# Kernel tuning notes

Hardware: AMD Instinct MI355X
Metric: run time of the kernel (lower is better)

## Reference

```python
import jax, jax.numpy as jnp
import numpy as np

B, S, D_IN, D_OUT, H = 4, 2048, 1024, 1024, 16
HD = D_OUT // H


def setup_inputs() -> dict:
    key = jax.random.key(0)
    ks = jax.random.split(key, 6)
    s_in = 1.0 / np.sqrt(D_IN)
    s_out = 1.0 / np.sqrt(D_OUT)
    return {
        "x": jax.random.normal(ks[0], (B, S, D_IN), dtype=jnp.float32),
        "W_q": jax.random.uniform(ks[1], (D_OUT, D_IN), jnp.float32, -s_in, s_in),
        "W_k": jax.random.uniform(ks[2], (D_OUT, D_IN), jnp.float32, -s_in, s_in),
        "W_v": jax.random.uniform(ks[3], (D_OUT, D_IN), jnp.float32, -s_in, s_in),
        "W_o": jax.random.uniform(ks[4], (D_OUT, D_OUT), jnp.float32, -s_out, s_out),
        "b_o": jax.random.uniform(ks[5], (D_OUT,), jnp.float32, -s_out, s_out),
    }


def reference(x, W_q, W_k, W_v, W_o, b_o):
    b, s, _ = x.shape
    # torch Linear: y = x @ W.T  (no qkv bias)
    q = (x @ W_q.T).reshape(b, s, H, HD).transpose(0, 2, 1, 3)  # [b,h,s,hd]
    k = (x @ W_k.T).reshape(b, s, H, HD).transpose(0, 2, 1, 3)
    v = (x @ W_v.T).reshape(b, s, H, HD).transpose(0, 2, 1, 3)
    scores = jnp.einsum("bhqd,bhkd->bhqk", q, k)  # [b,h,s,s]
    causal = jnp.triu(jnp.ones((s, s), dtype=bool), k=1)
    scores = jnp.where(causal, -jnp.inf, scores)
    attn = jax.nn.softmax(scores / np.sqrt(HD), axis=-1)
    # dropout p=0.0 -> identity
    ctx = jnp.einsum("bhqk,bhkd->bhqd", attn, v)  # [b,h,s,hd]
    ctx = ctx.transpose(0, 2, 1, 3).reshape(b, s, D_OUT)
    return ctx @ W_o.T + b_o
```

## Files before the change

### kernel.cpp

```cpp
#include <hip/hip_runtime.h>
#include <cstdint>
#include <cstddef>

#define S_LEN  2048
#define NHEAD  16
#define HDIM   64
#define KD     1024
#define BSROWS 8192

typedef __attribute__((ext_vector_type(4))) float          floatx4;
typedef __attribute__((ext_vector_type(8))) __bf16         bf16x8;
typedef __attribute__((ext_vector_type(8))) unsigned short ushort8v;
typedef __attribute__((ext_vector_type(4))) unsigned short ushort4v;
typedef __attribute__((ext_vector_type(4))) float          float4v;

__device__ __forceinline__ unsigned short f2bf(float f) {
  unsigned int u = __float_as_uint(f);
  u += 0x7fffu + ((u >> 16) & 1u);
  return (unsigned short)(u >> 16);
}

#if __has_builtin(__builtin_amdgcn_exp2f)
#define EXP2F(x) __builtin_amdgcn_exp2f(x)
#else
#define EXP2F(x) exp2f(x)
#endif

__device__ __forceinline__ unsigned int pack2bf(float a, float b) {
#if __has_builtin(__builtin_amdgcn_perm)
  return __builtin_amdgcn_perm(__float_as_uint(b), __float_as_uint(a), 0x07060302);
#else
  return (__float_as_uint(a) >> 16) | (__float_as_uint(b) & 0xffff0000u);
#endif
}

__device__ __forceinline__ void async_cp16(const void* gsrc, void* ldst) {
  __builtin_amdgcn_global_load_lds(
      (__attribute__((address_space(1))) void*)gsrc,
      (__attribute__((address_space(3))) void*)ldst,
      16, 0, 0);
}

#define XN4 2097152
#define WN4 262144

__global__ __launch_bounds__(256) void cvt_kernel(
    const float* __restrict__ x,  const float* __restrict__ wq,
    const float* __restrict__ wk, const float* __restrict__ wv,
    const float* __restrict__ wo,
    unsigned short* __restrict__ xb, unsigned short* __restrict__ wqkvb,
    unsigned short* __restrict__ wob)
{
  const int i = blockIdx.x * 256 + threadIdx.x;
  const float* src; unsigned short* dst; int off;
  if (i < XN4) { src = x; dst = xb; off = i; }
  else {
    const int j = i - XN4;
    if (j < WN4)          { src = wq; dst = wqkvb;           off = j; }
    else if (j < 2*WN4)   { src = wk; dst = wqkvb + 4*WN4;   off = j - WN4; }
    else if (j < 3*WN4)   { src = wv; dst = wqkvb + 8*WN4;   off = j - 2*WN4; }
    else                  { src = wo; dst = wob;             off = j - 3*WN4; }
  }
  const float4v v = ((const float4v*)src)[off];
  ushort4v o;
  o.x = f2bf(v.x); o.y = f2bf(v.y); o.z = f2bf(v.z); o.w = f2bf(v.w);
  ((ushort4v*)dst)[off] = o;
}

__device__ __forceinline__ void stage_j(
    int j, const unsigned short* __restrict__ gAs,
    const unsigned short* __restrict__ gBs,
    unsigned short* smem, const int wave)
{
  const int tk  = j >> 2, pos = j & 3;
  const int bufo = (tk & 1) << 15;
  const bool isA = (pos == 0) | (pos == 3);
  const int rowbase = (pos >= 2) ? 128 : 0;
  const unsigned short* g = (isA ? gAs : gBs) + (size_t)rowbase * KD + tk * 64;
  unsigned short* l = smem + bufo + (isA ? 0 : 16384) + rowbase * 64 + wave * 512;
  async_cp16(g,                  l);
  async_cp16(g + (size_t)64 * KD, l + 4096);
}

template<bool SWAP>
__device__ __forceinline__ void kloop256(
    const unsigned short* __restrict__ gAs,
    const unsigned short* __restrict__ gBs,
    unsigned short* smem, floatx4 (&acc)[8][4],
    const int wave, const int quad, const int l15)
{
  const int ar_base = (wave >> 2) * 64 + l15;
  const int br_base = (wave & 3) * 32 + l15;
  const int sw0 = ((quad)     ^ (l15 & 7)) * 8;
  const int sw1 = ((4 + quad) ^ (l15 & 7)) * 8;

  bf16x8 af[4][2];
  bf16x8 bfr[2][2][2];

#pragma unroll
  for (int j = 0; j < 6; ++j) stage_j(j, gAs, gBs, smem, wave);

#define LOADA(mh)                                                              \
  _Pragma("unroll") for (int mt = 0; mt < 4; ++mt) {                           \
    const unsigned short* ar = &As[((mh) * 128 + ar_base + mt * 16) * 64];     \
    af[mt][0] = *(const bf16x8*)(ar + sw0);                                    \
    af[mt][1] = *(const bf16x8*)(ar + sw1);                                    \
  }
#define LOADB(nh)                                                              \
  _Pragma("unroll") for (int nt = 0; nt < 2; ++nt) {                           \
    const unsigned short* br = &Bs[((nh) * 128 + br_base + nt * 16) * 64];     \
    bfr[nh][nt][0] = *(const bf16x8*)(br + sw0);                               \
    bfr[nh][nt][1] = *(const bf16x8*)(br + sw1);                               \
  }
#define MFMAQ(mh, nh)                                                          \
  __builtin_amdgcn_s_setprio(1);                                               \
  _Pragma("unroll") for (int mt = 0; mt < 4; ++mt)                             \
    _Pragma("unroll") for (int nt = 0; nt < 2; ++nt)                           \
      _Pragma("unroll") for (int ks = 0; ks < 2; ++ks) {                       \
        if (SWAP)                                                              \
          acc[(mh)*4+mt][(nh)*2+nt] = __builtin_amdgcn_mfma_f32_16x16x32_bf16( \
              bfr[nh][nt][ks], af[mt][ks], acc[(mh)*4+mt][(nh)*2+nt], 0,0,0);  \
        else                                                                   \
          acc[(mh)*4+mt][(nh)*2+nt] = __builtin_amdgcn_mfma_f32_16x16x32_bf16( \
              af[mt][ks], bfr[nh][nt][ks], acc[(mh)*4+mt][(nh)*2+nt], 0,0,0);  \
      }                                                                        \
  __builtin_amdgcn_s_setprio(0);

#pragma unroll 2
  for (int t = 0; t < 16; ++t) {
    const unsigned short* As = smem + ((t & 1) << 15);
    const unsigned short* Bs = As + 16384;
    const int j0 = 4 * t + 6;

    asm volatile("s_barrier" ::: "memory");
    if (j0 < 64) stage_j(j0, gAs, gBs, smem, wave);
    if (t < 15) asm volatile("s_waitcnt vmcnt(6)\n\ts_barrier" ::: "memory");
    else        asm volatile("s_waitcnt vmcnt(0)\n\ts_barrier" ::: "memory");
    LOADA(0)
    LOADB(0)
    MFMAQ(0, 0)

    asm volatile("s_barrier" ::: "memory");
    if (j0 + 1 < 64) stage_j(j0 + 1, gAs, gBs, smem, wave);
    LOADB(1)
    MFMAQ(0, 1)

    asm volatile("s_barrier" ::: "memory");
    if (j0 + 2 < 64) stage_j(j0 + 2, gAs, gBs, smem, wave);
    LOADA(1)
    MFMAQ(1, 0)

    asm volatile("s_barrier" ::: "memory");
    if (j0 + 3 < 64) stage_j(j0 + 3, gAs, gBs, smem, wave);
    MFMAQ(1, 1)
  }
#undef LOADA
#undef LOADB
#undef MFMAQ
}

__global__ __launch_bounds__(512, 2) void gemm_qkv8(
    const unsigned short* __restrict__ A,
    const unsigned short* __restrict__ Bw,
    unsigned short* __restrict__ Qo,
    unsigned short* __restrict__ Ko,
    unsigned short* __restrict__ Vto)
{
  __shared__ unsigned short smem[65536];
  const int tid  = threadIdx.x;
  const int wave = tid >> 6, lane = tid & 63;
  const int quad = lane >> 4, l15 = lane & 15;

  const int bid = (int)blockIdx.x;
  const int tau = (bid & 7) * 48 + (bid >> 3);
  const int m0 = (tau / 12) * 256, n0 = (tau % 12) * 256;

  const int strow = tid >> 3;
  const int stxc  = (tid & 7) ^ (strow & 7);
  const unsigned short* gAs = A  + (size_t)(m0 + strow) * KD + stxc * 8;
  const unsigned short* gBs = Bw + (size_t)(n0 + strow) * KD + stxc * 8;

  const floatx4 fzero = {0.f, 0.f, 0.f, 0.f};
  floatx4 acc[8][4];
#pragma unroll
  for (int i = 0; i < 8; i++)
#pragma unroll
    for (int j = 0; j < 4; j++) acc[i][j] = fzero;

  const int which = n0 >> 10;
  if (which < 2) kloop256<true >(gAs, gBs, smem, acc, wave, quad, l15);
  else           kloop256<false>(gAs, gBs, smem, acc, wave, quad, l15);

  const int h0 = (n0 & 1023) >> 6;
  const int b = m0 >> 11, sl = m0 & 2047;
  __syncthreads();

  if (which < 2) {
    unsigned short* dst = which ? Ko : Qo;
    const float scale = which ? 1.0f : 0.18033688011112042f;
#pragma unroll
    for (int mh = 0; mh < 2; ++mh) {
      if (mh) __syncthreads();
#pragma unroll
      for (int mt = 0; mt < 4; ++mt)
#pragma unroll
        for (int jn = 0; jn < 4; ++jn) {
          ushort4v t4;
#pragma unroll
          for (int r = 0; r < 4; ++r) t4[r] = f2bf(acc[mh * 4 + mt][jn][r] * scale);
          const int row = (wave >> 2) * 64 + mt * 16 + l15;
          const int col = (jn >> 1) * 128 + (wave & 3) * 32 + (jn & 1) * 16 + quad * 4;
          *(ushort4v*)&smem[row * 264 + col] = t4;
        }
      __syncthreads();
#pragma unroll
      for (int t8 = 0; t8 < 8; ++t8) {
        const int c = t8 * 512 + tid;
        const int sr = c >> 5, ch = c & 31;
        const int hs = ch >> 3, hd8 = (ch & 7) * 8;
        const ushort8v val = *(const ushort8v*)&smem[sr * 264 + hs * 64 + hd8];
        *(ushort8v*)&dst[((size_t)((b * NHEAD + h0 + hs) * S_LEN + sl + mh * 128 + sr)) * HDIM + hd8] = val;
      }
    }
  } else {
#pragma unroll
    for (int mh = 0; mh < 2; ++mh) {
      if (mh) __syncthreads();
#pragma unroll
      for (int mt = 0; mt < 4; ++mt)
#pragma unroll
        for (int jn = 0; jn < 4; ++jn) {
          ushort4v t4;
#pragma unroll
          for (int r = 0; r < 4; ++r) t4[r] = f2bf(acc[mh * 4 + mt][jn][r]);
          const int nl = (jn >> 1) * 128 + (wave & 3) * 32 + (jn & 1) * 16 + l15;
          const int sc = (wave >> 2) * 64 + mt * 16 + quad * 4;
          *(ushort4v*)&smem[nl * 136 + sc] = t4;
        }
      __syncthreads();
#pragma unroll
      for (int t8 = 0; t8 < 8; ++t8) {
        const int c = t8 * 512 + tid;
        const int nl = c >> 4, sc = (c & 15) * 8;
        const ushort8v val = *(const ushort8v*)&smem[nl * 136 + sc];
        *(ushort8v*)&Vto[((size_t)((b * NHEAD + h0 + (nl >> 6)) * HDIM + (nl & 63))) * S_LEN + sl + mh * 128 + sc] = val;
      }
    }
  }
}

template<bool SWAP>
__device__ __forceinline__ void kloop128(
    const unsigned short* __restrict__ gA,
    const unsigned short* __restrict__ gB,
    unsigned short* smem, floatx4 (&acc)[4][4],
    const int wave, const int quad, const int l15,
    const int wr, const int wc)
{
  {
    unsigned short* lA = smem + wave * 1024;
    unsigned short* lB = smem + 4096 + wave * 1024;
    async_cp16(gA,                    lA);
    async_cp16(gA + (size_t)16 * KD,  lA + 512);
    async_cp16(gB,                    lB);
    async_cp16(gB + (size_t)16 * KD,  lB + 512);
  }
  const int lsw = (l15 >> 1) & 3;

#pragma unroll 2
  for (int it = 0; it < 32; it++) {
    asm volatile("s_waitcnt vmcnt(0) lgkmcnt(0)\n\ts_barrier" ::: "memory");
    if (it + 1 < 32) {
      const int nb = (it + 1) & 1;
      const int ko = (it + 1) * 32;
      unsigned short* lA = smem + nb * 8192 + wave * 1024;
      unsigned short* lB = smem + nb * 8192 + 4096 + wave * 1024;
      async_cp16(gA + ko,                   lA);
      async_cp16(gA + ko + (size_t)16 * KD, lA + 512);
      async_cp16(gB + ko,                   lB);
      async_cp16(gB + ko + (size_t)16 * KD, lB + 512);
    }
    const unsigned short* As = smem + (it & 1) * 8192;
    const unsigned short* Bs = As + 4096;

    bf16x8 af[4], bfrag[4];
#pragma unroll
    for (int i = 0; i < 4; i++)
      af[i] = *(const bf16x8*)&As[(wr * 64 + i * 16 + l15) * 32 + (quad ^ lsw) * 8];
#pragma unroll
    for (int j = 0; j < 4; j++)
      bfrag[j] = *(const bf16x8*)&Bs[(wc * 64 + j * 16 + l15) * 32 + (quad ^ lsw) * 8];
#pragma unroll
    for (int i = 0; i < 4; i++)
#pragma unroll
      for (int j = 0; j < 4; j++) {
        if (SWAP)
          acc[i][j] = __builtin_amdgcn_mfma_f32_16x16x32_bf16(bfrag[j], af[i], acc[i][j], 0, 0, 0);
        else
          acc[i][j] = __builtin_amdgcn_mfma_f32_16x16x32_bf16(af[i], bfrag[j], acc[i][j], 0, 0, 0);
      }
  }
}

__global__ __launch_bounds__(512, 6) void attn_kernel(
    const unsigned short* __restrict__ Qg_,
    const unsigned short* __restrict__ Kg_,
    const unsigned short* __restrict__ Vtg_,
    unsigned short* __restrict__ CTX)
{
  __shared__ unsigned short smem[25088];
  const int tid  = threadIdx.x, wave = tid >> 6, lane = tid & 63;
  const int quad = lane >> 4, l15 = lane & 15;
  unsigned short* Pw = smem + 16384 + wave * 1088;

  const int bh = (int)blockIdx.x;
  const int yy = (int)blockIdx.y;
  const int qt = (yy < 4) ? yy : (yy < 8) ? (11 - yy) : (yy < 12) ? yy : (27 - yy);
  const int q0 = qt * 128;
  const size_t base = (size_t)bh * (S_LEN * HDIM);
  const unsigned short* Qg  = Qg_  + base;
  const unsigned short* Kg  = Kg_  + base;
  const unsigned short* Vtg = Vtg_ + base;
  const int qw = q0 + wave * 16;

  const int strow = lane >> 3;
  const int stxc  = (lane & 7) ^ strow;
  const unsigned short* kstage = Kg  + (size_t)(wave * 8 + strow) * HDIM  + stxc * 8;
  const unsigned short* vstage = Vtg + (size_t)(wave * 8 + strow) * S_LEN + stxc * 8;
  unsigned short* kd0 = smem + wave * 512;
  unsigned short* vd0 = smem + 4096 + wave * 512;

  async_cp16(kstage, kd0);
  async_cp16(vstage, vd0);

  bf16x8 qf[2];
#pragma unroll
  for (int ks = 0; ks < 2; ks++)
    qf[ks] = *(const bf16x8*)&Qg[(size_t)(qw + l15) * HDIM + ks * 32 + quad * 8];

  const int sw0 = ((quad)     ^ (l15 & 7)) * 8;
  const int sw1 = ((4 + quad) ^ (l15 & 7)) * 8;

  const floatx4 fzero = {0.f, 0.f, 0.f, 0.f};
  floatx4 O[4];
  float l_part = 0.f;
#pragma unroll
  for (int mt = 0; mt < 4; mt++) O[mt] = fzero;

  const int ntiles = 2 * qt + 2;

  for (int j = 0; j < ntiles; j++) {
    asm volatile("s_waitcnt vmcnt(0) lgkmcnt(0)\n\ts_barrier" ::: "memory");
    if (j + 1 < ntiles) {
      const int nb = (j + 1) & 1;
      async_cp16(kstage + (size_t)(j + 1) * 64 * HDIM, kd0 + nb * 8192);
      async_cp16(vstage + (size_t)(j + 1) * 64,        vd0 + nb * 8192);
    }
    const int k0 = j * 64;
    if (k0 > qw + 15) continue;
    const unsigned short* Ksb = smem + (j & 1) * 8192;
    const unsigned short* Vsb = Ksb + 4096;
    const int krel = qw + 15 - k0;

    floatx4 sa[4];
#pragma unroll
    for (int kt = 0; kt < 4; kt++) sa[kt] = fzero;
    __builtin_amdgcn_s_setprio(1);
#pragma unroll
    for (int kt = 0; kt < 4; kt++) {
      if (kt * 16 <= krel) {
        const unsigned short* kr = &Ksb[(kt * 16 + l15) * 64];
        sa[kt] = __builtin_amdgcn_mfma_f32_16x16x32_bf16(*(const bf16x8*)(kr + sw0), qf[0], sa[kt], 0, 0, 0);
        sa[kt] = __builtin_amdgcn_mfma_f32_16x16x32_bf16(*(const bf16x8*)(kr + sw1), qf[1], sa[kt], 0, 0, 0);
      }
    }
    __builtin_amdgcn_s_setprio(0);

    const int qrow = qw + l15;
#pragma unroll
    for (int kt = 0; kt < 4; kt++) {
      const int kbase = k0 + kt * 16;
      unsigned short* pdst = &Pw[l15 * 68 + kt * 16 + quad * 4];
      if (kt * 16 <= krel) {
        if (kbase + 15 > qw) {
#pragma unroll
          for (int r = 0; r < 4; r++)
            if (kbase + quad * 4 + r > qrow) sa[kt][r] = -INFINITY;
        }
        const float p0 = EXP2F(sa[kt][0]), p1 = EXP2F(sa[kt][1]);
        const float p2 = EXP2F(sa[kt][2]), p3 = EXP2F(sa[kt][3]);
        l_part += (p0 + p1) + (p2 + p3);
        uint2 pk; pk.x = pack2bf(p0, p1); pk.y = pack2bf(p2, p3);
        *(uint2*)pdst = pk;
      } else if ((kt >> 1) * 32 <= krel) {
        uint2 z; z.x = 0u; z.y = 0u;
        *(uint2*)pdst = z;
      }
    }
    asm volatile("s_waitcnt lgkmcnt(0)" ::: "memory");

#pragma unroll
    for (int ks = 0; ks < 2; ks++) {
      if (ks * 32 > krel) break;
      const unsigned short* ps = &Pw[l15 * 68 + ks * 32 + quad * 8];
      union { ushort4v h[2]; bf16x8 v; } pu;
      pu.h[0] = *(const ushort4v*)ps;
      pu.h[1] = *(const ushort4v*)(ps + 4);
      __builtin_amdgcn_s_setprio(1);
#pragma unroll
      for (int mt = 0; mt < 4; mt++) {
        const bf16x8 vf = *(const bf16x8*)(&Vsb[(mt * 16 + l15) * 64] + (ks ? sw1 : sw0));
        O[mt] = __builtin_amdgcn_mfma_f32_16x16x32_bf16(vf, pu.v, O[mt], 0, 0, 0);
      }
      __builtin_amdgcn_s_setprio(0);
    }
  }

#pragma unroll
  for (int d = 16; d < 64; d <<= 1)
    l_part += __shfl_xor(l_part, d, 64);

  {
    const float inv = 1.0f / l_part;
#pragma unroll
    for (int mt = 0; mt < 4; mt++)
#pragma unroll
      for (int a = 0; a < 2; a++) {
        const unsigned int pk =
            (unsigned int)f2bf(O[mt][2 * a] * inv) |
            ((unsigned int)f2bf(O[mt][2 * a + 1] * inv) << 16);
        *(unsigned int*)&Pw[l15 * 68 + mt * 16 + quad * 4 + 2 * a] = pk;
      }
  }
  asm volatile("s_waitcnt lgkmcnt(0)" ::: "memory");
  const int b = bh >> 4, h = bh & 15;
#pragma unroll
  for (int it = 0; it < 2; it++) {
    const int g = it * 64 + lane;
    const int row = g >> 3, c8 = (g & 7) * 8;
    union { ushort4v h[2]; ushort8v v; } ou;
    ou.h[0] = *(const ushort4v*)&Pw[row * 68 + c8];
    ou.h[1] = *(const ushort4v*)&Pw[row * 68 + c8 + 4];
    const int s = qw + row;
    *(ushort8v*)&CTX[((size_t)(b * S_LEN + s)) * KD + h * HDIM + c8] = ou.v;
  }
}

__global__ __launch_bounds__(256) void gemm_out(
    const unsigned short* __restrict__ A,
    const unsigned short* __restrict__ Bw,
    const float* __restrict__ bias,
    float* __restrict__ out)
{
  __shared__ unsigned short smem[16384];
  const int tid  = threadIdx.x;
  const int wave = tid >> 6, lane = tid & 63;
  const int quad = lane >> 4, l15 = lane & 15;
  const int wr = wave >> 1, wc = wave & 1;
  const int m0 = blockIdx.x * 128, n0 = blockIdx.y * 128;

  const int srow = lane >> 2;
  const int scol = ((lane & 3) ^ ((srow >> 1) & 3)) * 8;
  const unsigned short* gA = A  + (size_t)(m0 + wave * 32 + srow) * KD + scol;
  const unsigned short* gB = Bw + (size_t)(n0 + wave * 32 + srow) * KD + scol;

  const floatx4 fzero = {0.f, 0.f, 0.f, 0.f};
  floatx4 acc[4][4];
#pragma unroll
  for (int i = 0; i < 4; i++)
#pragma unroll
    for (int j = 0; j < 4; j++) acc[i][j] = fzero;

  kloop128<true>(gA, gB, smem, acc, wave, quad, l15, wr, wc);

#pragma unroll
  for (int j = 0; j < 4; j++) {
    const int nb4 = n0 + wc * 64 + j * 16 + quad * 4;
    const float4v bb = *(const float4v*)&bias[nb4];
#pragma unroll
    for (int i = 0; i < 4; i++) {
      const int m = m0 + wr * 64 + i * 16 + l15;
      float4v st;
#pragma unroll
      for (int r = 0; r < 4; r++) st[r] = acc[i][j][r] + bb[r];
      *(float4v*)&out[(size_t)m * KD + nb4] = st;
    }
  }
}

extern "C" void kernel_launch(void* const* d_in, const int* in_sizes, int n_in,
                              void* d_out, int out_size, void* d_ws, size_t ws_size,
                              hipStream_t stream) {
  (void)in_sizes; (void)n_in; (void)out_size;
  const float* x  = (const float*)d_in[0];
  const float* wq = (const float*)d_in[1];
  const float* wk = (const float*)d_in[2];
  const float* wv = (const float*)d_in[3];
  const float* wo = (const float*)d_in[4];
  const float* bo = (const float*)d_in[5];
  float* out = (float*)d_out;

  if (ws_size < (size_t)92274688) return;
  char* ws = (char*)d_ws;
  unsigned short* xb    = (unsigned short*)(ws);
  unsigned short* wqkvb = (unsigned short*)(ws + (size_t)16777216);
  unsigned short* wob   = (unsigned short*)(ws + (size_t)23068672);
  unsigned short* qws   = (unsigned short*)(ws + (size_t)25165824);
  unsigned short* kws   = (unsigned short*)(ws + (size_t)41943040);
  unsigned short* vtws  = (unsigned short*)(ws + (size_t)58720256);
  unsigned short* ctxws = (unsigned short*)(ws + (size_t)75497472);

  cvt_kernel<<<12288, 256, 0, stream>>>(x, wq, wk, wv, wo, xb, wqkvb, wob);
  gemm_qkv8<<<384, 512, 0, stream>>>(xb, wqkvb, qws, kws, vtws);
  attn_kernel<<<dim3(64, 16), 512, 0, stream>>>(qws, kws, vtws, ctxws);
  gemm_out<<<dim3(64, 8), 256, 0, stream>>>(ctxws, wob, bo, out);
}
```

Before: 230.3 us.

## Shrink QKV GEMM tile to 128x256 and double grid to 768 blocks

```diff
diff --git a/kernel.cpp b/kernel.cpp
--- a/kernel.cpp
+++ b/kernel.cpp
@@ -67,113 +67,109 @@
   ((ushort4v*)dst)[off] = o;
 }
 
-__device__ __forceinline__ void stage_j(
-    int j, const unsigned short* __restrict__ gAs,
+__device__ __forceinline__ void stage_h12(
+    const int h, const int tk,
+    const unsigned short* __restrict__ gAs,
     const unsigned short* __restrict__ gBs,
     unsigned short* smem, const int wave)
 {
-  const int tk  = j >> 2, pos = j & 3;
-  const int bufo = (tk & 1) << 15;
-  const bool isA = (pos == 0) | (pos == 3);
-  const int rowbase = (pos >= 2) ? 128 : 0;
-  const unsigned short* g = (isA ? gAs : gBs) + (size_t)rowbase * KD + tk * 64;
-  unsigned short* l = smem + bufo + (isA ? 0 : 16384) + rowbase * 64 + wave * 512;
-  async_cp16(g,                  l);
+  const int bufo = (tk & 1) * 24576;
+  const unsigned short* g;
+  unsigned short* l;
+  if (h == 0)      { g = gAs + tk * 64;                      l = smem + bufo + wave * 512; }
+  else if (h == 1) { g = gBs + tk * 64;                      l = smem + bufo + 8192  + wave * 512; }
+  else             { g = gBs + (size_t)128 * KD + tk * 64;   l = smem + bufo + 16384 + wave * 512; }
+  async_cp16(g,                   l);
   async_cp16(g + (size_t)64 * KD, l + 4096);
 }
 
 template<bool SWAP>
-__device__ __forceinline__ void kloop256(
+__device__ __forceinline__ void kloop12(
     const unsigned short* __restrict__ gAs,
     const unsigned short* __restrict__ gBs,
-    unsigned short* smem, floatx4 (&acc)[8][4],
+    unsigned short* smem, floatx4 (&acc)[4][4],
     const int wave, const int quad, const int l15)
 {
   const int ar_base = (wave >> 2) * 64 + l15;
-  const int br_base = (wave & 3) * 32 + l15;
+  const int bc_base = (wave & 3) * 64 + l15;
   const int sw0 = ((quad)     ^ (l15 & 7)) * 8;
   const int sw1 = ((4 + quad) ^ (l15 & 7)) * 8;
 
   bf16x8 af[4][2];
-  bf16x8 bfr[2][2][2];
-
-#pragma unroll
-  for (int j = 0; j < 6; ++j) stage_j(j, gAs, gBs, smem, wave);
-
-#define LOADA(mh)                                                              \
-  _Pragma("unroll") for (int mt = 0; mt < 4; ++mt) {                           \
-    const unsigned short* ar = &As[((mh) * 128 + ar_base + mt * 16) * 64];     \
-    af[mt][0] = *(const bf16x8*)(ar + sw0);                                    \
-    af[mt][1] = *(const bf16x8*)(ar + sw1);                                    \
-  }
-#define LOADB(nh)                                                              \
-  _Pragma("unroll") for (int nt = 0; nt < 2; ++nt) {                           \
-    const unsigned short* br = &Bs[((nh) * 128 + br_base + nt * 16) * 64];     \
-    bfr[nh][nt][0] = *(const bf16x8*)(br + sw0);                               \
-    bfr[nh][nt][1] = *(const bf16x8*)(br + sw1);                               \
-  }
-#define MFMAQ(mh, nh)                                                          \
+  bf16x8 bfr[2][2];
+
+  stage_h12(0, 0, gAs, gBs, smem, wave);
+  stage_h12(1, 0, gAs, gBs, smem, wave);
+  stage_h12(2, 0, gAs, gBs, smem, wave);
+
+#define MFMAQ12(nh)                                                            \
   __builtin_amdgcn_s_setprio(1);                                               \
   _Pragma("unroll") for (int mt = 0; mt < 4; ++mt)                             \
     _Pragma("unroll") for (int nt = 0; nt < 2; ++nt)                           \
       _Pragma("unroll") for (int ks = 0; ks < 2; ++ks) {                       \
         if (SWAP)                                                              \
-          acc[(mh)*4+mt][(nh)*2+nt] = __builtin_amdgcn_mfma_f32_16x16x32_bf16( \
-              bfr[nh][nt][ks], af[mt][ks], acc[(mh)*4+mt][(nh)*2+nt], 0,0,0);  \
+          acc[mt][(nh)*2+nt] = __builtin_amdgcn_mfma_f32_16x16x32_bf16(        \
+              bfr[nt][ks], af[mt][ks], acc[mt][(nh)*2+nt], 0, 0, 0);           \
         else                                                                   \
-          acc[(mh)*4+mt][(nh)*2+nt] = __builtin_amdgcn_mfma_f32_16x16x32_bf16( \
-              af[mt][ks], bfr[nh][nt][ks], acc[(mh)*4+mt][(nh)*2+nt], 0,0,0);  \
+          acc[mt][(nh)*2+nt] = __builtin_amdgcn_mfma_f32_16x16x32_bf16(        \
+              af[mt][ks], bfr[nt][ks], acc[mt][(nh)*2+nt], 0, 0, 0);           \
       }                                                                        \
   __builtin_amdgcn_s_setprio(0);
 
 #pragma unroll 2
   for (int t = 0; t < 16; ++t) {
-    const unsigned short* As = smem + ((t & 1) << 15);
-    const unsigned short* Bs = As + 16384;
-    const int j0 = 4 * t + 6;
+    const unsigned short* As = smem + (t & 1) * 24576;
+    const unsigned short* Bs = As + 8192;
 
     asm volatile("s_barrier" ::: "memory");
-    if (j0 < 64) stage_j(j0, gAs, gBs, smem, wave);
-    if (t < 15) asm volatile("s_waitcnt vmcnt(6)\n\ts_barrier" ::: "memory");
+    if (t + 1 < 16) {
+      stage_h12(0, t + 1, gAs, gBs, smem, wave);
+      stage_h12(1, t + 1, gAs, gBs, smem, wave);
+    }
+    if (t < 15) asm volatile("s_waitcnt vmcnt(4)\n\ts_barrier" ::: "memory");
     else        asm volatile("s_waitcnt vmcnt(0)\n\ts_barrier" ::: "memory");
-    LOADA(0)
-    LOADB(0)
-    MFMAQ(0, 0)
+#pragma unroll
+    for (int mt = 0; mt < 4; ++mt) {
+      const unsigned short* ar = &As[(ar_base + mt * 16) * 64];
+      af[mt][0] = *(const bf16x8*)(ar + sw0);
+      af[mt][1] = *(const bf16x8*)(ar + sw1);
+    }
+#pragma unroll
+    for (int nt = 0; nt < 2; ++nt) {
+      const unsigned short* br = &Bs[(bc_base + nt * 16) * 64];
+      bfr[nt][0] = *(const bf16x8*)(br + sw0);
+      bfr[nt][1] = *(const bf16x8*)(br + sw1);
+    }
+    MFMAQ12(0)
 
     asm volatile("s_barrier" ::: "memory");
-    if (j0 + 1 < 64) stage_j(j0 + 1, gAs, gBs, smem, wave);
-    LOADB(1)
-    MFMAQ(0, 1)
-
-    asm volatile("s_barrier" ::: "memory");
-    if (j0 + 2 < 64) stage_j(j0 + 2, gAs, gBs, smem, wave);
-    LOADA(1)
-    MFMAQ(1, 0)
-
-    asm volatile("s_barrier" ::: "memory");
-    if (j0 + 3 < 64) stage_j(j0 + 3, gAs, gBs, smem, wave);
-    MFMAQ(1, 1)
-  }
-#undef LOADA
-#undef LOADB
-#undef MFMAQ
-}
-
-__global__ __launch_bounds__(512, 2) void gemm_qkv8(
+    if (t + 1 < 16) stage_h12(2, t + 1, gAs, gBs, smem, wave);
+#pragma unroll
+    for (int nt = 0; nt < 2; ++nt) {
+      const unsigned short* br = &Bs[(bc_base + 32 + nt * 16) * 64];
+      bfr[nt][0] = *(const bf16x8*)(br + sw0);
+      bfr[nt][1] = *(const bf16x8*)(br + sw1);
+    }
+    MFMAQ12(1)
+  }
+#undef MFMAQ12
+}
+
+__global__ __launch_bounds__(512, 2) void gemm_qkv12(
     const unsigned short* __restrict__ A,
     const unsigned short* __restrict__ Bw,
     unsigned short* __restrict__ Qo,
     unsigned short* __restrict__ Ko,
     unsigned short* __restrict__ Vto)
 {
-  __shared__ unsigned short smem[65536];
+  __shared__ unsigned short smem[49152];
   const int tid  = threadIdx.x;
   const int wave = tid >> 6, lane = tid & 63;
   const int quad = lane >> 4, l15 = lane & 15;
 
   const int bid = (int)blockIdx.x;
-  const int tau = (bid & 7) * 48 + (bid >> 3);
-  const int m0 = (tau / 12) * 256, n0 = (tau % 12) * 256;
+  const int tau = (bid & 7) * 96 + (bid >> 3);
+  const int m0 = (tau / 12) * 128, n0 = (tau % 12) * 256;
 
   const int strow = tid >> 3;
   const int stxc  = (tid & 7) ^ (strow & 7);
@@ -181,15 +177,15 @@
   const unsigned short* gBs = Bw + (size_t)(n0 + strow) * KD + stxc * 8;
 
   const floatx4 fzero = {0.f, 0.f, 0.f, 0.f};
-  floatx4 acc[8][4];
-#pragma unroll
-  for (int i = 0; i < 8; i++)
+  floatx4 acc[4][4];
+#pragma unroll
+  for (int i = 0; i < 4; i++)
 #pragma unroll
     for (int j = 0; j < 4; j++) acc[i][j] = fzero;
 
   const int which = n0 >> 10;
-  if (which < 2) kloop256<true >(gAs, gBs, smem, acc, wave, quad, l15);
-  else           kloop256<false>(gAs, gBs, smem, acc, wave, quad, l15);
+  if (which < 2) kloop12<true >(gAs, gBs, smem, acc, wave, quad, l15);
+  else           kloop12<false>(gAs, gBs, smem, acc, wave, quad, l15);
 
   const int h0 = (n0 & 1023) >> 6;
   const int b = m0 >> 11, sl = m0 & 2047;
@@ -199,52 +195,44 @@
     unsigned short* dst = which ? Ko : Qo;
     const float scale = which ? 1.0f : 0.18033688011112042f;
 #pragma unroll
-    for (int mh = 0; mh < 2; ++mh) {
-      if (mh) __syncthreads();
-#pragma unroll
-      for (int mt = 0; mt < 4; ++mt)
-#pragma unroll
-        for (int jn = 0; jn < 4; ++jn) {
-          ushort4v t4;
-#pragma unroll
-          for (int r = 0; r < 4; ++r) t4[r] = f2bf(acc[mh * 4 + mt][jn][r] * scale);
-          const int row = (wave >> 2) * 64 + mt * 16 + l15;
-          const int col = (jn >> 1) * 128 + (wave & 3) * 32 + (jn & 1) * 16 + quad * 4;
-          *(ushort4v*)&smem[row * 264 + col] = t4;
-        }
-      __syncthreads();
-#pragma unroll
-      for (int t8 = 0; t8 < 8; ++t8) {
-        const int c = t8 * 512 + tid;
-        const int sr = c >> 5, ch = c & 31;
-        const int hs = ch >> 3, hd8 = (ch & 7) * 8;
-        const ushort8v val = *(const ushort8v*)&smem[sr * 264 + hs * 64 + hd8];
-        *(ushort8v*)&dst[((size_t)((b * NHEAD + h0 + hs) * S_LEN + sl + mh * 128 + sr)) * HDIM + hd8] = val;
-      }
+    for (int mt = 0; mt < 4; ++mt)
+#pragma unroll
+      for (int jn = 0; jn < 4; ++jn) {
+        ushort4v t4;
+#pragma unroll
+        for (int r = 0; r < 4; ++r) t4[r] = f2bf(acc[mt][jn][r] * scale);
+        const int row = (wave >> 2) * 64 + mt * 16 + l15;
+        const int col = (wave & 3) * 64 + (jn >> 1) * 32 + (jn & 1) * 16 + quad * 4;
+        *(ushort4v*)&smem[row * 264 + col] = t4;
+      }
+    __syncthreads();
+#pragma unroll
+    for (int t8 = 0; t8 < 8; ++t8) {
+      const int c = t8 * 512 + tid;
+      const int sr = c >> 5, ch = c & 31;
+      const int hs = ch >> 3, hd8 = (ch & 7) * 8;
+      const ushort8v val = *(const ushort8v*)&smem[sr * 264 + hs * 64 + hd8];
+      *(ushort8v*)&dst[((size_t)((b * NHEAD + h0 + hs) * S_LEN + sl + sr)) * HDIM + hd8] = val;
     }
   } else {
 #pragma unroll
-    for (int mh = 0; mh < 2; ++mh) {
-      if (mh) __syncthreads();
-#pragma unroll
-      for (int mt = 0; mt < 4; ++mt)
-#pragma unroll
-        for (int jn = 0; jn < 4; ++jn) {
-          ushort4v t4;
-#pragma unroll
-          for (int r = 0; r < 4; ++r) t4[r] = f2bf(acc[mh * 4 + mt][jn][r]);
-          const int nl = (jn >> 1) * 128 + (wave & 3) * 32 + (jn & 1) * 16 + l15;
-          const int sc = (wave >> 2) * 64 + mt * 16 + quad * 4;
-          *(ushort4v*)&smem[nl * 136 + sc] = t4;
-        }
-      __syncthreads();
-#pragma unroll
-      for (int t8 = 0; t8 < 8; ++t8) {
-        const int c = t8 * 512 + tid;
-        const int nl = c >> 4, sc = (c & 15) * 8;
-        const ushort8v val = *(const ushort8v*)&smem[nl * 136 + sc];
-        *(ushort8v*)&Vto[((size_t)((b * NHEAD + h0 + (nl >> 6)) * HDIM + (nl & 63))) * S_LEN + sl + mh * 128 + sc] = val;
-      }
+    for (int mt = 0; mt < 4; ++mt)
+#pragma unroll
+      for (int jn = 0; jn < 4; ++jn) {
+        ushort4v t4;
+#pragma unroll
+        for (int r = 0; r < 4; ++r) t4[r] = f2bf(acc[mt][jn][r]);
+        const int nl = (wave & 3) * 64 + (jn >> 1) * 32 + (jn & 1) * 16 + l15;
+        const int sc = (wave >> 2) * 64 + mt * 16 + quad * 4;
+        *(ushort4v*)&smem[nl * 136 + sc] = t4;
+      }
+    __syncthreads();
+#pragma unroll
+    for (int t8 = 0; t8 < 8; ++t8) {
+      const int c = t8 * 512 + tid;
+      const int nl = c >> 4, sc8 = (c & 15) * 8;
+      const ushort8v val = *(const ushort8v*)&smem[nl * 136 + sc8];
+      *(ushort8v*)&Vto[((size_t)((b * NHEAD + h0 + (nl >> 6)) * HDIM + (nl & 63))) * S_LEN + sl + sc8] = val;
     }
   }
 }
@@ -511,7 +499,7 @@
   unsigned short* ctxws = (unsigned short*)(ws + (size_t)75497472);
 
   cvt_kernel<<<12288, 256, 0, stream>>>(x, wq, wk, wv, wo, xb, wqkvb, wob);
-  gemm_qkv8<<<384, 512, 0, stream>>>(xb, wqkvb, qws, kws, vtws);
+  gemm_qkv12<<<768, 512, 0, stream>>>(xb, wqkvb, qws, kws, vtws);
   attn_kernel<<<dim3(64, 16), 512, 0, stream>>>(qws, kws, vtws, ctxws);
   gemm_out<<<dim3(64, 8), 256, 0, stream>>>(ctxws, wob, bo, out);
 }
```

Result: slower. 239.2 us (+3.9%).
